# Performance work log

Hardware: AMD Instinct MI355X
Metric: run time of the kernel (lower is better)

The kernel has to match this reference:

```python
import jax, jax.numpy as jnp
import numpy as np

N_NODES = 50000
F_IN = 128
F_OUT = 128
N_REL = 8
N_BASIS = 4
N_EDGES = 500000  # per relation


def setup_inputs() -> dict:
    key = jax.random.key(0)
    k1, k2, k3, k4, k5, k6 = jax.random.split(key, 6)
    x = jax.random.normal(k1, (N_NODES, F_IN), dtype=jnp.float32)
    # glorot-style scale for basis weights
    scale = np.sqrt(6.0 / (F_IN + F_OUT)).astype(np.float32)
    W_basis = jax.random.uniform(k2, (N_BASIS, F_IN, F_OUT), dtype=jnp.float32, minval=-scale, maxval=scale)
    cscale = np.sqrt(6.0 / (N_REL + N_BASIS)).astype(np.float32)
    W_comp = jax.random.uniform(k3, (N_REL, N_BASIS), dtype=jnp.float32, minval=-cscale, maxval=cscale)
    edge_vals = jax.random.uniform(k4, (N_REL, N_EDGES), dtype=jnp.float32)
    edge_src = jax.random.randint(k5, (N_REL, N_EDGES), 0, N_NODES, dtype=jnp.int32)
    edge_dst = jax.random.randint(k6, (N_REL, N_EDGES), 0, N_NODES, dtype=jnp.int32)
    return {"x": x, "W_basis": W_basis, "W_comp": W_comp,
            "edge_vals": edge_vals, "edge_src": edge_src, "edge_dst": edge_dst}


def reference(x, W_basis, W_comp, edge_vals, edge_src, edge_dst):
    # Basis mixing: per-relation weight W_r = sum_b comp[r,b] * W_basis[b]
    W_rel = jnp.einsum('rb,bio->rio', W_comp, W_basis)          # [R, Fin, Fout]
    # Dense transform per relation: pre_sup_r = x @ W_r
    pre = jnp.einsum('nf,rfo->rno', x, W_rel)                   # [R, N, Fout]
    n = x.shape[0]
    out = jnp.zeros((n, W_basis.shape[-1]), dtype=x.dtype)
    # SpMM per relation as gather + scatter-add, accumulated (tf.add_n)
    for r in range(W_comp.shape[0]):
        msg = edge_vals[r][:, None] * pre[r, edge_src[r]]       # [E, Fout]
        out = out + jax.ops.segment_sum(msg, edge_dst[r], num_segments=n)
    return jax.nn.relu(out)
```

## Files before the change

### kernel.cpp

```cpp
#include <hip/hip_runtime.h>

#define F 128
#define NB 4
#define NR 8
#define KPB 512
#define BCAP 6144
#define EPB 16384
#define MAXBKT 784
#define CAPW 384

typedef __attribute__((ext_vector_type(8))) short bf16x8;
typedef __attribute__((ext_vector_type(4))) float f32x4;
typedef __attribute__((ext_vector_type(2))) float f32x2;
typedef unsigned long long u64;

__device__ __forceinline__ unsigned f2bf(float f) {
    unsigned u = __float_as_uint(f);
    return (u + 0x7FFFu + ((u >> 16) & 1u)) >> 16;
}
__device__ __forceinline__ unsigned f2bf2(float lo, float hi) {
    return f2bf(lo) | (f2bf(hi) << 16);
}

__global__ void cvt_x_kernel(const float4* __restrict__ x4, uint4* __restrict__ xb, int total8) {
    int i = blockIdx.x * blockDim.x + threadIdx.x;
    if (i >= total8) return;
    float4 a = x4[(size_t)i * 2], b = x4[(size_t)i * 2 + 1];
    xb[i] = make_uint4(f2bf2(a.x, a.y), f2bf2(a.z, a.w), f2bf2(b.x, b.y), f2bf2(b.z, b.w));
}

__global__ void cvt_w_kernel(const float* __restrict__ Wb, unsigned short* __restrict__ Bt) {
    int t = blockIdx.x * blockDim.x + threadIdx.x;
    if (t >= F * NB * F) return;
    int o = t >> 9, bk = t & 511, b = bk >> 7, k = bk & 127;
    Bt[t] = (unsigned short)f2bf(Wb[((size_t)b * F + k) * F + o]);
}

__global__ void init_gcur(int* __restrict__ gcur, int nbkt) {
    int i = blockIdx.x * blockDim.x + threadIdx.x;
    if (i < nbkt) gcur[i] = i * BCAP;
}

__global__ __launch_bounds__(1024) void bucket_scatter(const int* __restrict__ es,
                                                       const float* __restrict__ ev,
                                                       const int* __restrict__ ed,
                                                       int* __restrict__ gcur,
                                                       u64* __restrict__ bbuf,
                                                       int E, int nbkt) {
    __shared__ int lcnt[MAXBKT];
    __shared__ int lbase[MAXBKT];
    const int r = blockIdx.y;
    const int e0 = blockIdx.x * EPB;
    const int e1 = min(e0 + EPB, E);
    const size_t ebase = (size_t)r * E;
    const int t = threadIdx.x;
    const int bbuf_end = nbkt * BCAP - 1;

    for (int i = t; i < nbkt; i += 1024) lcnt[i] = 0;
    __syncthreads();

    int dd[16];
#pragma unroll
    for (int k = 0; k < 4; ++k) {
        int base = e0 + k * 4096 + t * 4;
        if (base + 4 <= e1) {
            int4 d4 = *(const int4*)&ed[ebase + base];
            dd[k * 4 + 0] = d4.x; dd[k * 4 + 1] = d4.y;
            dd[k * 4 + 2] = d4.z; dd[k * 4 + 3] = d4.w;
        } else {
            dd[k * 4 + 0] = -1; dd[k * 4 + 1] = -1;
            dd[k * 4 + 2] = -1; dd[k * 4 + 3] = -1;
        }
    }
#pragma unroll
    for (int k = 0; k < 16; ++k)
        if (dd[k] >= 0) atomicAdd(&lcnt[(dd[k] * NR + r) >> 9], 1);
    __syncthreads();

    for (int i = t; i < nbkt; i += 1024) {
        int c = lcnt[i];
        lbase[i] = c ? atomicAdd(&gcur[i], c) : 0;
        lcnt[i] = 0;
    }
    __syncthreads();

#pragma unroll
    for (int k = 0; k < 4; ++k) {
        int base = e0 + k * 4096 + t * 4;
        if (base + 4 <= e1) {
            int4 s4 = *(const int4*)&es[ebase + base];
            float4 v4 = *(const float4*)&ev[ebase + base];
            int ss[4] = {s4.x, s4.y, s4.z, s4.w};
            float vv[4] = {v4.x, v4.y, v4.z, v4.w};
#pragma unroll
            for (int u = 0; u < 4; ++u) {
                int key = dd[k * 4 + u] * NR + r;
                int b = key >> 9;
                int rk = atomicAdd(&lcnt[b], 1);
                int pos = min(lbase[b] + rk, bbuf_end);
                bbuf[pos] = (u64)((unsigned)(ss[u] & 0xFFFF) | ((unsigned)(key & 511) << 16))
                          | ((u64)(f2bf(vv[u]) << 16) << 32);
            }
        }
    }
}

__global__ void bt_kernel(const int* __restrict__ gcur, int* __restrict__ bt, int nbkt) {
    int i = blockIdx.x * blockDim.x + threadIdx.x;
    if (i < nbkt) bt[i] = gcur[i] - i * BCAP;
}

__global__ __launch_bounds__(512) void scan_reduce(const int* __restrict__ cnt,
                                                   int* __restrict__ bsum, int M) {
    int base = blockIdx.x * 4096 + threadIdx.x * 8;
    int s = 0;
    if (base + 8 <= M) {
        int4 a = *(const int4*)&cnt[base];
        int4 c = *(const int4*)&cnt[base + 4];
        s = a.x + a.y + a.z + a.w + c.x + c.y + c.z + c.w;
    } else {
        for (int i = base; i < M; ++i) s += cnt[i];
    }
    for (int off = 1; off < 64; off <<= 1) s += __shfl_xor(s, off);
    __shared__ int wsum[8];
    if ((threadIdx.x & 63) == 0) wsum[threadIdx.x >> 6] = s;
    __syncthreads();
    if (threadIdx.x == 0) {
        int t = 0;
#pragma unroll
        for (int k = 0; k < 8; ++k) t += wsum[k];
        bsum[blockIdx.x] = t;
    }
}

__global__ __launch_bounds__(1024) void scan_bsums(const int* __restrict__ bsum,
                                                   int* __restrict__ bbase, int nb) {
    __shared__ int sums[1024];
    int t = threadIdx.x;
    int v = (t < nb) ? bsum[t] : 0;
    sums[t] = v;
    __syncthreads();
    for (int d = 1; d < 1024; d <<= 1) {
        int u = (t >= d) ? sums[t - d] : 0;
        __syncthreads();
        sums[t] += u;
        __syncthreads();
    }
    if (t < nb) bbase[t] = sums[t] - v;
}

__global__ __launch_bounds__(512) void scan_write(const int* __restrict__ cnt,
                                                  const int* __restrict__ bbase,
                                                  int* __restrict__ offs, int M) {
    int t = threadIdx.x;
    int base = blockIdx.x * 4096 + t * 8;
    int ex[8];
    int s = 0;
    if (base + 8 <= M) {
        int4 a = *(const int4*)&cnt[base];
        int4 c = *(const int4*)&cnt[base + 4];
        int tmp[8] = {a.x, a.y, a.z, a.w, c.x, c.y, c.z, c.w};
#pragma unroll
        for (int k = 0; k < 8; ++k) { ex[k] = s; s += tmp[k]; }
    } else {
        for (int k = 0; k < 8; ++k) ex[k] = 0;
        int s2 = 0;
        for (int i = base, k = 0; i < M; ++i, ++k) { ex[k] = s2; s2 += cnt[i]; }
        s = s2;
    }
    __shared__ int sums[512];
    sums[t] = s;
    __syncthreads();
    for (int d = 1; d < 512; d <<= 1) {
        int u = (t >= d) ? sums[t - d] : 0;
        __syncthreads();
        sums[t] += u;
        __syncthreads();
    }
    int tb = bbase[blockIdx.x] + ((t == 0) ? 0 : sums[t - 1]);
    if (base + 8 <= M) {
        *(int4*)&offs[base] = make_int4(tb + ex[0], tb + ex[1], tb + ex[2], tb + ex[3]);
        *(int4*)&offs[base + 4] = make_int4(tb + ex[4], tb + ex[5], tb + ex[6], tb + ex[7]);
    } else {
        for (int i = base, k = 0; i < M; ++i, ++k) offs[i] = tb + ex[k];
    }
}

__global__ __launch_bounds__(512) void densify(const u64* __restrict__ bbuf,
                                               const int* __restrict__ gcur,
                                               const int* __restrict__ boff,
                                               unsigned* __restrict__ payload,
                                               unsigned* __restrict__ segdesc, int M) {
    __shared__ int kcnt[KPB];
    __shared__ int koff[KPB];
    __shared__ int kcur[KPB];
    __shared__ int stmp[KPB];
    const int bk = blockIdx.x;
    const int start = bk * BCAP;
    const int cntE = min(gcur[bk] - start, BCAP);
    const int t = threadIdx.x;
    kcnt[t] = 0;
    kcur[t] = 0;
    __syncthreads();
    for (int i = t; i < cntE; i += 512) {
        u64 e = bbuf[start + i];
        atomicAdd(&kcnt[((unsigned)e >> 16) & 511], 1);
    }
    __syncthreads();
    stmp[t] = kcnt[t];
    __syncthreads();
    for (int d = 1; d < KPB; d <<= 1) {
        int v = (t >= d) ? stmp[t - d] : 0;
        __syncthreads();
        stmp[t] += v;
        __syncthreads();
    }
    koff[t] = stmp[t] - kcnt[t];
    __syncthreads();
    const int gb = boff[bk];
    int key = bk * KPB + t;
    if (key < M)
        segdesc[key] = ((unsigned)(gb + koff[t]) << 8) | (unsigned)min(kcnt[t], 255);
    for (int i = t; i < cntE; i += 512) {
        u64 e = bbuf[start + i];
        unsigned elo = (unsigned)e;
        int klo = (elo >> 16) & 511;
        int rk = atomicAdd(&kcur[klo], 1);
        payload[gb + koff[klo] + rk] = (elo & 0xFFFFu) | (unsigned)(e >> 32);
    }
}

__global__ __launch_bounds__(256) void accum_kernel(const unsigned* __restrict__ xb,
                                                    const unsigned* __restrict__ payload,
                                                    const unsigned* __restrict__ segdesc,
                                                    const float* __restrict__ comp,
                                                    unsigned* __restrict__ mix,
                                                    int c0, int c1) {
    __shared__ float4 scomp[NR];
    __shared__ unsigned plds[4 * CAPW];
    if (threadIdx.x < NR) scomp[threadIdx.x] = ((const float4*)comp)[threadIdx.x];
    __syncthreads();
    int wave = threadIdx.x >> 6, lane = threadIdx.x & 63;
    int d = c0 + blockIdx.x * 4 + wave;
    if (d >= c1) return;

    uint4 sA = *(const uint4*)&segdesc[(size_t)d * 8];
    uint4 sB = *(const uint4*)&segdesc[(size_t)d * 8 + 4];
    unsigned s0 = (unsigned)__builtin_amdgcn_readfirstlane((int)sA.x);
    unsigned s1 = (unsigned)__builtin_amdgcn_readfirstlane((int)sA.y);
    unsigned s2 = (unsigned)__builtin_amdgcn_readfirstlane((int)sA.z);
    unsigned s3 = (unsigned)__builtin_amdgcn_readfirstlane((int)sA.w);
    unsigned s4 = (unsigned)__builtin_amdgcn_readfirstlane((int)sB.x);
    unsigned s5 = (unsigned)__builtin_amdgcn_readfirstlane((int)sB.y);
    unsigned s6 = (unsigned)__builtin_amdgcn_readfirstlane((int)sB.z);
    unsigned s7 = (unsigned)__builtin_amdgcn_readfirstlane((int)sB.w);
    const unsigned start = s0 >> 8;
    const int b0 = (int)((s1 >> 8) - start);
    const int b1 = (int)((s2 >> 8) - start);
    const int b2 = (int)((s3 >> 8) - start);
    const int b3 = (int)((s4 >> 8) - start);
    const int b4 = (int)((s5 >> 8) - start);
    const int b5 = (int)((s6 >> 8) - start);
    const int b6 = (int)((s7 >> 8) - start);
    const int b7 = (int)((s7 >> 8) - start + (s7 & 255u));
    const int total = b7;
    auto bval = [&](int c) {
        return c == 0 ? b0 : c == 1 ? b1 : c == 2 ? b2 : c == 3 ? b3
             : c == 4 ? b4 : c == 5 ? b5 : c == 6 ? b6 : b7;
    };

    const unsigned lbase = wave * CAPW;
    const int stg = min(total, CAPW);
    for (int o = lane; o < stg; o += 64)
        plds[lbase + o] = __builtin_nontemporal_load(&payload[start + o]);

    f32x2 a0 = {0.f, 0.f}, a1 = {0.f, 0.f}, a2 = {0.f, 0.f}, a3 = {0.f, 0.f};
    f32x2 sr = {0.f, 0.f};
    int cur = 0;
    int nb = bval(0);
    auto flush = [&]() {
        float4 cw = scomp[cur];
        a0 += sr * cw.x;
        a1 += sr * cw.y;
        a2 += sr * cw.z;
        a3 += sr * cw.w;
        sr = (f32x2){0.f, 0.f};
        ++cur;
        nb = bval(cur < 7 ? cur : 7);
    };

    int i = 0;
    for (; i + 8 <= total; i += 8) {
        unsigned pw[8];
        if (i + 8 <= CAPW) {
#pragma unroll
            for (int k = 0; k < 8; ++k)
                pw[k] = (unsigned)__builtin_amdgcn_readfirstlane((int)plds[lbase + i + k]);
        } else {
#pragma unroll
            for (int k = 0; k < 8; ++k)
                pw[k] = (unsigned)__builtin_amdgcn_readfirstlane((int)payload[start + i + k]);
        }
        unsigned g[8];
#pragma unroll
        for (int k = 0; k < 8; ++k)
            g[k] = xb[(size_t)(pw[k] & 0xFFFFu) * 64 + lane];
#pragma unroll
        for (int k = 0; k < 8; ++k) {
            while (i + k >= nb && cur < 7) flush();
            float v = __uint_as_float(pw[k] & 0xFFFF0000u);
            f32x2 xv = {__uint_as_float(g[k] << 16), __uint_as_float(g[k] & 0xFFFF0000u)};
            sr += xv * v;
        }
    }
    for (; i < total; ++i) {
        unsigned pw = (unsigned)__builtin_amdgcn_readfirstlane(
            (int)((i < CAPW) ? plds[lbase + i] : payload[start + i]));
        unsigned g = xb[(size_t)(pw & 0xFFFFu) * 64 + lane];
        while (i >= nb && cur < 7) flush();
        float v = __uint_as_float(pw & 0xFFFF0000u);
        f32x2 xv = {__uint_as_float(g << 16), __uint_as_float(g & 0xFFFF0000u)};
        sr += xv * v;
    }
    while (cur < 8) {
        float4 cw = scomp[cur];
        a0 += sr * cw.x;
        a1 += sr * cw.y;
        a2 += sr * cw.z;
        a3 += sr * cw.w;
        sr = (f32x2){0.f, 0.f};
        ++cur;
    }

    unsigned* mrow = mix + (size_t)(d - c0) * 256 + lane;
    mrow[0]   = f2bf2(a0.x, a0.y);
    mrow[64]  = f2bf2(a1.x, a1.y);
    mrow[128] = f2bf2(a2.x, a2.y);
    mrow[192] = f2bf2(a3.x, a3.y);
}

__global__ __launch_bounds__(256) void gemm_mfma(const unsigned short* __restrict__ mix,
                                                 const unsigned short* __restrict__ Bt,
                                                 float* __restrict__ out,
                                                 int rows, int gbase, int N) {
    __shared__ unsigned short As[128 * 64];
    __shared__ unsigned short Bs[128 * 64];
    const int t = threadIdx.x;
    const int row0 = blockIdx.x * 128;
    const int w = t >> 6, lane = t & 63;
    f32x4 acc[2][8] = {};

    for (int kt = 0; kt < 8; ++kt) {
        __syncthreads();
        for (int u = t; u < 1024; u += 256) {
            int r = u >> 3, c = u & 7;
            int k8 = c * 8;
            int ks = k8 ^ ((r & 7) << 3);
            uint4 av = make_uint4(0, 0, 0, 0);
            if (row0 + r < rows) av = *(const uint4*)&mix[(size_t)(row0 + r) * 512 + kt * 64 + k8];
            *(uint4*)&As[r * 64 + ks] = av;
            uint4 bv = *(const uint4*)&Bt[(size_t)r * 512 + kt * 64 + k8];
            *(uint4*)&Bs[r * 64 + ks] = bv;
        }
        __syncthreads();
#pragma unroll
        for (int ks = 0; ks < 2; ++ks) {
            bf16x8 a[2], b[8];
            const int kbase = ks * 32 + (lane >> 4) * 8;
#pragma unroll
            for (int i = 0; i < 2; ++i) {
                int r = w * 32 + i * 16 + (lane & 15);
                int kk = kbase ^ ((r & 7) << 3);
                a[i] = *(bf16x8*)&As[r * 64 + kk];
            }
#pragma unroll
            for (int jj = 0; jj < 8; ++jj) {
                int o = jj * 16 + (lane & 15);
                int kk = kbase ^ ((o & 7) << 3);
                b[jj] = *(bf16x8*)&Bs[o * 64 + kk];
            }
#pragma unroll
            for (int i = 0; i < 2; ++i)
#pragma unroll
                for (int jj = 0; jj < 8; ++jj)
                    acc[i][jj] = __builtin_amdgcn_mfma_f32_16x16x32_bf16(a[i], b[jj], acc[i][jj], 0, 0, 0);
        }
    }

#pragma unroll
    for (int i = 0; i < 2; ++i) {
        int mbase = w * 32 + i * 16 + (lane >> 4) * 4;
#pragma unroll
        for (int q = 0; q < 4; ++q) {
            int m = mbase + q;
            int gr = gbase + row0 + m;
            if (row0 + m < rows && gr < N) {
#pragma unroll
                for (int jj = 0; jj < 8; ++jj) {
                    int n = jj * 16 + (lane & 15);
                    out[(size_t)gr * F + n] = fmaxf(acc[i][jj][q], 0.f);
                }
            }
        }
    }
}

extern "C" void kernel_launch(void* const* d_in, const int* in_sizes, int n_in,
                              void* d_out, int out_size, void* d_ws, size_t ws_size,
                              hipStream_t stream) {
    const float* x  = (const float*)d_in[0];
    const float* Wb = (const float*)d_in[1];
    const float* Wc = (const float*)d_in[2];
    const float* ev = (const float*)d_in[3];
    const int*   es = (const int*)d_in[4];
    const int*   ed = (const int*)d_in[5];
    float* out = (float*)d_out;

    const int N = in_sizes[0] / F;
    const int E = in_sizes[3] / NR;
    const int M = NR * N;
    const int nbkt = (M + KPB - 1) / KPB;
    const int nb2 = (nbkt + 4095) / 4096;

    char* p = (char*)d_ws;
    auto alloc = [&](size_t bytes) -> char* {
        char* q = p;
        p += (bytes + 255) & ~(size_t)255;
        return q;
    };
    u64* bbuf          = (u64*)alloc((size_t)nbkt * BCAP * 8);
    unsigned* payload  = (unsigned*)alloc((size_t)NR * E * 4);
    int* gcur          = (int*)alloc((size_t)nbkt * 4);
    int* bt            = (int*)alloc((size_t)nbkt * 4);
    int* bsum          = (int*)alloc((size_t)(nb2 + 16) * 4);
    int* bbase         = (int*)alloc((size_t)(nb2 + 16) * 4);
    int* boff          = (int*)alloc((size_t)nbkt * 4);
    unsigned* segdesc  = (unsigned*)alloc((size_t)M * 4);
    unsigned short* Bt = (unsigned short*)alloc((size_t)F * NB * F * 2);
    unsigned* xb       = (unsigned*)alloc((size_t)N * F * 2);

    size_t used = (size_t)(p - (char*)d_ws);
    size_t rem = ws_size > used ? ws_size - used : (size_t)(128 * 1024);
    size_t mix_rows = (rem / (512 * 2)) & ~(size_t)127;
    int chunk = (int)(mix_rows < 128 ? 128
                      : (mix_rows > (size_t)N ? (size_t)((N + 127) & ~(size_t)127) : mix_rows));
    unsigned short* mixbuf = (unsigned short*)p;

    cvt_x_kernel<<<(N * F / 8 + 255) / 256, 256, 0, stream>>>((const float4*)x, (uint4*)xb, N * F / 8);
    cvt_w_kernel<<<(F * NB * F + 255) / 256, 256, 0, stream>>>(Wb, Bt);
    init_gcur<<<(nbkt + 255) / 256, 256, 0, stream>>>(gcur, nbkt);

    dim3 bg((E + EPB - 1) / EPB, NR);
    bucket_scatter<<<bg, 1024, 0, stream>>>(es, ev, ed, gcur, bbuf, E, nbkt);

    bt_kernel<<<(nbkt + 255) / 256, 256, 0, stream>>>(gcur, bt, nbkt);
    scan_reduce<<<nb2, 512, 0, stream>>>(bt, bsum, nbkt);
    scan_bsums<<<1, 1024, 0, stream>>>(bsum, bbase, nb2);
    scan_write<<<nb2, 512, 0, stream>>>(bt, bbase, boff, nbkt);

    densify<<<nbkt, 512, 0, stream>>>(bbuf, gcur, boff, payload, segdesc, M);

    for (int c0 = 0; c0 < N; c0 += chunk) {
        int crows = min(chunk, N - c0);
        accum_kernel<<<(crows + 3) / 4, 256, 0, stream>>>(xb, payload, segdesc, Wc,
                                                          (unsigned*)mixbuf, c0, c0 + crows);
        gemm_mfma<<<(crows + 127) / 128, 256, 0, stream>>>(mixbuf, Bt, out, crows, c0, N);
    }
}
```

Before: 229.0 us.

## Sort edges by bucket in LDS before coalesced global scatter; cache buckets in densify

bucket_scatter now loads all edge fields up front and computes a local prefix over per-bucket counts. It places the packed entries into a shared-memory array ordered by bucket, then writes them to the global bucket buffer in contiguous runs instead of scattered 8-byte stores. The bucket id is packed into the high word so the write-out pass can find each entry's global base. densify caches its bucket's entries in LDS so the second pass does not re-read global memory. In exchange, the block size halves and LDS use grows (64KB plus 48KB), which may lower occupancy, and the edge tile per block shrinks.

```diff
diff --git a/kernel.cpp b/kernel.cpp
--- a/kernel.cpp
+++ b/kernel.cpp
@@ -5,7 +5,7 @@
 #define NR 8
 #define KPB 512
 #define BCAP 6144
-#define EPB 16384
+#define EPB 8192
 #define MAXBKT 784
 #define CAPW 384
 
@@ -41,35 +41,49 @@
     if (i < nbkt) gcur[i] = i * BCAP;
 }
 
-__global__ __launch_bounds__(1024) void bucket_scatter(const int* __restrict__ es,
-                                                       const float* __restrict__ ev,
-                                                       const int* __restrict__ ed,
-                                                       int* __restrict__ gcur,
-                                                       u64* __restrict__ bbuf,
-                                                       int E, int nbkt) {
+__global__ __launch_bounds__(512) void bucket_scatter(const int* __restrict__ es,
+                                                      const float* __restrict__ ev,
+                                                      const int* __restrict__ ed,
+                                                      int* __restrict__ gcur,
+                                                      u64* __restrict__ bbuf,
+                                                      int E, int nbkt) {
+    __shared__ u64 sorted[EPB];
     __shared__ int lcnt[MAXBKT];
+    __shared__ int lofs[MAXBKT];
     __shared__ int lbase[MAXBKT];
+    __shared__ int stmp[512];
     const int r = blockIdx.y;
     const int e0 = blockIdx.x * EPB;
     const int e1 = min(e0 + EPB, E);
+    const int cnt = e1 - e0;
     const size_t ebase = (size_t)r * E;
     const int t = threadIdx.x;
     const int bbuf_end = nbkt * BCAP - 1;
 
-    for (int i = t; i < nbkt; i += 1024) lcnt[i] = 0;
-    __syncthreads();
-
-    int dd[16];
+    for (int i = t; i < nbkt; i += 512) lcnt[i] = 0;
+    __syncthreads();
+
+    int dd[16], ss[16];
+    float vv[16];
 #pragma unroll
     for (int k = 0; k < 4; ++k) {
-        int base = e0 + k * 4096 + t * 4;
+        int base = e0 + k * 2048 + t * 4;
         if (base + 4 <= e1) {
             int4 d4 = *(const int4*)&ed[ebase + base];
-            dd[k * 4 + 0] = d4.x; dd[k * 4 + 1] = d4.y;
-            dd[k * 4 + 2] = d4.z; dd[k * 4 + 3] = d4.w;
+            int4 s4 = *(const int4*)&es[ebase + base];
+            float4 v4 = *(const float4*)&ev[ebase + base];
+            dd[k * 4 + 0] = d4.x; dd[k * 4 + 1] = d4.y; dd[k * 4 + 2] = d4.z; dd[k * 4 + 3] = d4.w;
+            ss[k * 4 + 0] = s4.x; ss[k * 4 + 1] = s4.y; ss[k * 4 + 2] = s4.z; ss[k * 4 + 3] = s4.w;
+            vv[k * 4 + 0] = v4.x; vv[k * 4 + 1] = v4.y; vv[k * 4 + 2] = v4.z; vv[k * 4 + 3] = v4.w;
         } else {
-            dd[k * 4 + 0] = -1; dd[k * 4 + 1] = -1;
-            dd[k * 4 + 2] = -1; dd[k * 4 + 3] = -1;
+#pragma unroll
+            for (int u = 0; u < 4; ++u) {
+                int idx = base + u;
+                bool ok = idx < e1;
+                dd[k * 4 + u] = ok ? ed[ebase + idx] : -1;
+                ss[k * 4 + u] = ok ? es[ebase + idx] : 0;
+                vv[k * 4 + u] = ok ? ev[ebase + idx] : 0.f;
+            }
         }
     }
 #pragma unroll
@@ -77,31 +91,42 @@
         if (dd[k] >= 0) atomicAdd(&lcnt[(dd[k] * NR + r) >> 9], 1);
     __syncthreads();
 
-    for (int i = t; i < nbkt; i += 1024) {
-        int c = lcnt[i];
-        lbase[i] = c ? atomicAdd(&gcur[i], c) : 0;
-        lcnt[i] = 0;
-    }
-    __syncthreads();
-
-#pragma unroll
-    for (int k = 0; k < 4; ++k) {
-        int base = e0 + k * 4096 + t * 4;
-        if (base + 4 <= e1) {
-            int4 s4 = *(const int4*)&es[ebase + base];
-            float4 v4 = *(const float4*)&ev[ebase + base];
-            int ss[4] = {s4.x, s4.y, s4.z, s4.w};
-            float vv[4] = {v4.x, v4.y, v4.z, v4.w};
-#pragma unroll
-            for (int u = 0; u < 4; ++u) {
-                int key = dd[k * 4 + u] * NR + r;
-                int b = key >> 9;
-                int rk = atomicAdd(&lcnt[b], 1);
-                int pos = min(lbase[b] + rk, bbuf_end);
-                bbuf[pos] = (u64)((unsigned)(ss[u] & 0xFFFF) | ((unsigned)(key & 511) << 16))
-                          | ((u64)(f2bf(vv[u]) << 16) << 32);
-            }
-        }
+    int c0v = (2 * t < nbkt) ? lcnt[2 * t] : 0;
+    int c1v = (2 * t + 1 < nbkt) ? lcnt[2 * t + 1] : 0;
+    stmp[t] = c0v + c1v;
+    __syncthreads();
+    for (int d = 1; d < 512; d <<= 1) {
+        int v = (t >= d) ? stmp[t - d] : 0;
+        __syncthreads();
+        stmp[t] += v;
+        __syncthreads();
+    }
+    int pre = (t == 0) ? 0 : stmp[t - 1];
+    if (2 * t < nbkt) lofs[2 * t] = pre;
+    if (2 * t + 1 < nbkt) lofs[2 * t + 1] = pre + c0v;
+    for (int b = t; b < nbkt; b += 512) {
+        int c = lcnt[b];
+        lbase[b] = c ? atomicAdd(&gcur[b], c) : 0;
+        lcnt[b] = 0;
+    }
+    __syncthreads();
+
+#pragma unroll
+    for (int k = 0; k < 16; ++k) {
+        if (dd[k] < 0) continue;
+        int key = dd[k] * NR + r;
+        int b = key >> 9;
+        int rk = atomicAdd(&lcnt[b], 1);
+        sorted[lofs[b] + rk] = (u64)((unsigned)(ss[k] & 0xFFFF) | ((unsigned)(key & 511) << 16))
+                             | ((u64)((f2bf(vv[k]) << 16) | (unsigned)b) << 32);
+    }
+    __syncthreads();
+
+    for (int i = t; i < cnt; i += 512) {
+        u64 e = sorted[i];
+        int bid = (int)((unsigned)(e >> 32) & 0x3FFu);
+        int tgt = min(lbase[bid] + (i - lofs[bid]), bbuf_end);
+        bbuf[tgt] = e;
     }
 }
 
@@ -191,6 +216,8 @@
                                                const int* __restrict__ boff,
                                                unsigned* __restrict__ payload,
                                                unsigned* __restrict__ segdesc, int M) {
+    __shared__ unsigned slo[BCAP];
+    __shared__ unsigned shi[BCAP];
     __shared__ int kcnt[KPB];
     __shared__ int koff[KPB];
     __shared__ int kcur[KPB];
@@ -204,7 +231,10 @@
     __syncthreads();
     for (int i = t; i < cntE; i += 512) {
         u64 e = bbuf[start + i];
-        atomicAdd(&kcnt[((unsigned)e >> 16) & 511], 1);
+        unsigned elo = (unsigned)e;
+        slo[i] = elo;
+        shi[i] = (unsigned)(e >> 32);
+        atomicAdd(&kcnt[(elo >> 16) & 511], 1);
     }
     __syncthreads();
     stmp[t] = kcnt[t];
@@ -222,11 +252,10 @@
     if (key < M)
         segdesc[key] = ((unsigned)(gb + koff[t]) << 8) | (unsigned)min(kcnt[t], 255);
     for (int i = t; i < cntE; i += 512) {
-        u64 e = bbuf[start + i];
-        unsigned elo = (unsigned)e;
+        unsigned elo = slo[i];
         int klo = (elo >> 16) & 511;
         int rk = atomicAdd(&kcur[klo], 1);
-        payload[gb + koff[klo] + rk] = (elo & 0xFFFFu) | (unsigned)(e >> 32);
+        payload[gb + koff[klo] + rk] = (elo & 0xFFFFu) | (shi[i] & 0xFFFF0000u);
     }
 }
 
@@ -451,7 +480,7 @@
     init_gcur<<<(nbkt + 255) / 256, 256, 0, stream>>>(gcur, nbkt);
 
     dim3 bg((E + EPB - 1) / EPB, NR);
-    bucket_scatter<<<bg, 1024, 0, stream>>>(es, ev, ed, gcur, bbuf, E, nbkt);
+    bucket_scatter<<<bg, 512, 0, stream>>>(es, ev, ed, gcur, bbuf, E, nbkt);
 
     bt_kernel<<<(nbkt + 255) / 256, 256, 0, stream>>>(gcur, bt, nbkt);
     scan_reduce<<<nb2, 512, 0, stream>>>(bt, bsum, nbkt);
```

After: 211.8 us. 1.08x faster.
